# Optimization experiments

Measured on AMD Instinct MI355X. Metric: run time of the kernel, lower is better.

Reference implementation:

```python
import jax, jax.numpy as jnp
import numpy as np

HEADS = 8
DIM_HEAD = 64
SCALE = DIM_HEAD ** -0.5


def setup_inputs() -> dict:
    key = jax.random.key(0)
    ks = jax.random.split(key, 8)
    B, Nq, Dq = 4, 2048, 512
    Nk, Dc = 1024, 768
    inner = HEADS * DIM_HEAD  # 512
    x = jax.random.normal(ks[0], (B, Nq, Dq), dtype=jnp.float32)
    context = jax.random.normal(ks[1], (B, Nk, Dc), dtype=jnp.float32)
    # Linear weights stored [in, out]; y = x @ W (+ b)
    Wq = jax.random.normal(ks[2], (Dq, inner), dtype=jnp.float32) / np.sqrt(Dq)
    Wk = jax.random.normal(ks[3], (Dc, inner), dtype=jnp.float32) / np.sqrt(Dc)
    Wv = jax.random.normal(ks[4], (Dc, inner), dtype=jnp.float32) / np.sqrt(Dc)
    Wo = jax.random.normal(ks[5], (inner, Dq), dtype=jnp.float32) / np.sqrt(inner)
    bo = jax.random.normal(ks[6], (Dq,), dtype=jnp.float32) * 0.01
    return {"x": x, "context": context, "Wq": Wq, "Wk": Wk, "Wv": Wv, "Wo": Wo, "bo": bo}


def reference(x, context, Wq, Wk, Wv, Wo, bo):
    B, Nq, _ = x.shape
    Nk = context.shape[1]
    # projections
    q = x @ Wq          # [B, Nq, h*d]
    k = context @ Wk    # [B, Nk, h*d]
    v = context @ Wv    # [B, Nk, h*d]
    # split heads: b n (h d) -> b h n d
    q = q.reshape(B, Nq, HEADS, DIM_HEAD).transpose(0, 2, 1, 3)
    k = k.reshape(B, Nk, HEADS, DIM_HEAD).transpose(0, 2, 1, 3)
    v = v.reshape(B, Nk, HEADS, DIM_HEAD).transpose(0, 2, 1, 3)
    # fp32 QK^T (ATTN_PRECISION == 'fp32' path)
    sim = jnp.einsum('bhid,bhjd->bhij', q.astype(jnp.float32), k.astype(jnp.float32)) * SCALE
    attn = jax.nn.softmax(sim, axis=-1)
    out = jnp.einsum('bhij,bhjd->bhid', attn, v)  # [B, h, Nq, d]
    out = out.transpose(0, 2, 1, 3).reshape(B, Nq, HEADS * DIM_HEAD)
    return out @ Wo + bo  # dropout=0 -> identity
```

## Files before the change

kernel.cpp:

```cpp
#include <hip/hip_runtime.h>
#include <cstddef>
#include <cstdint>

typedef __attribute__((ext_vector_type(8))) short bf16x8;
typedef __attribute__((ext_vector_type(4))) float f32x4;

static __device__ __forceinline__ short f2bf(float f) {
    union { float f; unsigned u; } x;
    x.f = f;
    unsigned r = (x.u + 0x7FFFu + ((x.u >> 16) & 1u)) >> 16;
    return (short)r;
}

typedef __attribute__((address_space(3))) unsigned lds_u;
typedef const __attribute__((address_space(1))) unsigned glb_u;
static __device__ __forceinline__ void gld_lds16(const void* g, void* l) {
    __builtin_amdgcn_global_load_lds((glb_u*)g, (lds_u*)l, 16, 0, 0);
}

__global__ __launch_bounds__(256) void convert_kernel(
    const float* __restrict__ x, const float* __restrict__ c,
    short* __restrict__ xb, short* __restrict__ cb, int n1, int n2)
{
    int i = blockIdx.x * 256 + threadIdx.x;
    int nn1 = n1 >> 2;
    const float* src; short* dst; int off;
    if (i < nn1) { src = x; dst = xb; off = i; }
    else { src = c; dst = cb; off = i - nn1; if (off >= (n2 >> 2)) return; }
    float4 v = ((const float4*)src)[off];
    ushort4 w;
    w.x = (unsigned short)f2bf(v.x); w.y = (unsigned short)f2bf(v.y);
    w.z = (unsigned short)f2bf(v.z); w.w = (unsigned short)f2bf(v.w);
    ((ushort4*)dst)[off] = w;
}

__global__ __launch_bounds__(256) void wtrans_kernel(
    const float* __restrict__ Wq, const float* __restrict__ Wk,
    const float* __restrict__ Wv, const float* __restrict__ Wo,
    short* __restrict__ wqT, short* __restrict__ wkvT, short* __restrict__ woT)
{
    __shared__ float T[32][33];
    const int z = blockIdx.z;
    const float* src; short* dst; int R;
    if (z == 0)      { src = Wq; dst = wqT;  R = 512; }
    else if (z == 1) { src = Wk; dst = wkvT; R = 768; }
    else if (z == 2) { src = Wv; dst = wkvT + (size_t)512 * 768; R = 768; }
    else             { src = Wo; dst = woT;  R = 512; }
    const int yt = blockIdx.y;
    if (yt * 32 >= R) return;
    const int xt = blockIdx.x;
    const int tid = threadIdx.x;
    {
        int r = tid >> 3, c4 = (tid & 7) * 4;
        float4 v = *(const float4*)&src[(size_t)(yt * 32 + r) * 512 + xt * 32 + c4];
        T[r][c4] = v.x; T[r][c4 + 1] = v.y; T[r][c4 + 2] = v.z; T[r][c4 + 3] = v.w;
    }
    __syncthreads();
    {
        int cc = tid >> 3, r4 = (tid & 7) * 4;
        ushort4 w;
        w.x = (unsigned short)f2bf(T[r4][cc]);     w.y = (unsigned short)f2bf(T[r4 + 1][cc]);
        w.z = (unsigned short)f2bf(T[r4 + 2][cc]); w.w = (unsigned short)f2bf(T[r4 + 3][cc]);
        *(ushort4*)&dst[(size_t)(xt * 32 + cc) * R + yt * 32 + r4] = w;
    }
}

__global__ __launch_bounds__(256) void vtrans_kernel(
    const short* __restrict__ v, short* __restrict__ vT)
{
    __shared__ short T[32][33];
    const int b = blockIdx.z, yt = blockIdx.y, xt = blockIdx.x;
    const int tid = threadIdx.x;
    {
        int r = tid >> 3, c4 = (tid & 7) * 4;
        ushort4 vv = *(const ushort4*)&v[((size_t)(b * 1024 + yt * 32 + r)) * 1024 + xt * 32 + c4];
        T[r][c4] = (short)vv.x; T[r][c4 + 1] = (short)vv.y;
        T[r][c4 + 2] = (short)vv.z; T[r][c4 + 3] = (short)vv.w;
    }
    __syncthreads();
    {
        int cc = tid >> 3, r4 = (tid & 7) * 4;
        ushort4 w;
        w.x = (unsigned short)T[r4][cc];     w.y = (unsigned short)T[r4 + 1][cc];
        w.z = (unsigned short)T[r4 + 2][cc]; w.w = (unsigned short)T[r4 + 3][cc];
        *(ushort4*)&vT[((size_t)(b * 512 + xt * 32 + cc)) * 1024 + yt * 32 + r4] = w;
    }
}

static __device__ __forceinline__ void gemm_core(
    const short* __restrict__ A, const short* __restrict__ BT, int K,
    int bm, int bn, short* As, short* Bs, f32x4 acc[4][4])
{
    const int tid  = threadIdx.x;
    const int lane = tid & 63;
    const int wave = tid >> 6;
    const int lm   = lane & 15;
    const int quad = lane >> 4;
    const int wm = (wave >> 1) * 64;
    const int wn = (wave & 1) * 64;
    const int c = tid >> 7, r = tid & 127;

    {
        const short* Ag = &A[(size_t)(bm + r) * K];
        const short* Bg = &BT[(size_t)(bn + r) * K];
        gld_lds16(Ag + c * 8,       &As[tid * 8]);
        gld_lds16(Ag + (c + 2) * 8, &As[(tid + 256) * 8]);
        gld_lds16(Bg + c * 8,       &Bs[tid * 8]);
        gld_lds16(Bg + (c + 2) * 8, &Bs[(tid + 256) * 8]);
    }

    for (int k0 = 0, it = 0; k0 < K; k0 += 32, ++it) {
        short* Ac = As + (it & 1) * 4096;
        short* Bc = Bs + (it & 1) * 4096;
        __syncthreads();
        if (k0 + 32 < K) {
            short* An = As + ((it & 1) ^ 1) * 4096;
            short* Bn = Bs + ((it & 1) ^ 1) * 4096;
            const short* Ag = &A[(size_t)(bm + r) * K + k0 + 32];
            const short* Bg = &BT[(size_t)(bn + r) * K + k0 + 32];
            gld_lds16(Ag + c * 8,       &An[tid * 8]);
            gld_lds16(Ag + (c + 2) * 8, &An[(tid + 256) * 8]);
            gld_lds16(Bg + c * 8,       &Bn[tid * 8]);
            gld_lds16(Bg + (c + 2) * 8, &Bn[(tid + 256) * 8]);
        }
        bf16x8 af[4], bfr[4];
        #pragma unroll
        for (int i = 0; i < 4; ++i)
            af[i] = *(const bf16x8*)&Ac[(quad * 128 + wm + i * 16 + lm) * 8];
        #pragma unroll
        for (int j = 0; j < 4; ++j)
            bfr[j] = *(const bf16x8*)&Bc[(quad * 128 + wn + j * 16 + lm) * 8];
        #pragma unroll
        for (int i = 0; i < 4; ++i)
            #pragma unroll
            for (int j = 0; j < 4; ++j)
                acc[i][j] = __builtin_amdgcn_mfma_f32_16x16x32_bf16(
                    af[i], bfr[j], acc[i][j], 0, 0, 0);
    }
}

__global__ __launch_bounds__(256) void qkv_kernel(
    const short* __restrict__ xb, const short* __restrict__ cb,
    const short* __restrict__ wqT, const short* __restrict__ wkvT,
    short* __restrict__ qb, short* __restrict__ kvb)
{
    __shared__ short As[2 * 4096];
    __shared__ short Bs[2 * 4096];
    const int bid = blockIdx.x;
    const short *A, *BT; short* C; int K, ldc, bm, bn;
    if (bid < 256) { A = xb; BT = wqT;  C = qb;  K = 512; ldc = 512;
                     bm = (bid >> 2) * 128; bn = (bid & 3) * 128; }
    else { int b2 = bid - 256; A = cb; BT = wkvT; C = kvb; K = 768; ldc = 1024;
           bm = (b2 >> 3) * 128; bn = (b2 & 7) * 128; }

    f32x4 acc[4][4] = {};
    gemm_core(A, BT, K, bm, bn, As, Bs, acc);

    const int lane = threadIdx.x & 63, wave = threadIdx.x >> 6;
    const int lm = lane & 15, quad = lane >> 4;
    const int wm = (wave >> 1) * 64, wn = (wave & 1) * 64;
    #pragma unroll
    for (int j = 0; j < 4; ++j) {
        int col = bn + wn + j * 16 + lm;
        #pragma unroll
        for (int i = 0; i < 4; ++i) {
            int row0 = bm + wm + i * 16 + quad * 4;
            #pragma unroll
            for (int r = 0; r < 4; ++r)
                C[(size_t)(row0 + r) * ldc + col] = f2bf(acc[i][j][r]);
        }
    }
}

__global__ __launch_bounds__(256) void ogemm_kernel(
    const short* __restrict__ ob, const short* __restrict__ woT,
    const float* __restrict__ bias, float* __restrict__ out)
{
    __shared__ short As[2 * 4096];
    __shared__ short Bs[2 * 4096];
    const int bid = blockIdx.x;
    const int bm = (bid >> 2) * 128, bn = (bid & 3) * 128;

    f32x4 acc[4][4] = {};
    gemm_core(ob, woT, 512, bm, bn, As, Bs, acc);

    const int lane = threadIdx.x & 63, wave = threadIdx.x >> 6;
    const int lm = lane & 15, quad = lane >> 4;
    const int wm = (wave >> 1) * 64, wn = (wave & 1) * 64;
    #pragma unroll
    for (int j = 0; j < 4; ++j) {
        int col = bn + wn + j * 16 + lm;
        float bv = bias[col];
        #pragma unroll
        for (int i = 0; i < 4; ++i) {
            int row0 = bm + wm + i * 16 + quad * 4;
            #pragma unroll
            for (int r = 0; r < 4; ++r)
                out[(size_t)(row0 + r) * 512 + col] = acc[i][j][r] + bv;
        }
    }
}

__global__ __launch_bounds__(256) void attn_kernel(
    const short* __restrict__ q, const short* __restrict__ k,
    const short* __restrict__ vT, short* __restrict__ o)
{
    __shared__ short Qs[4096];
    __shared__ short Ks[2 * 4096];
    __shared__ short Vs[2 * 4096];

    const int tid  = threadIdx.x;
    const int lane = tid & 63;
    const int wave = tid >> 6;
    const int lm   = lane & 15;
    const int quad = lane >> 4;
    const int qt = blockIdx.x, h = blockIdx.y, b = blockIdx.z;
    const size_t qrow0 = (size_t)b * 2048 + qt * 64;
    const size_t krow0 = (size_t)b * 1024;
    const int hcol = h * 64;
    const size_t vrow0 = ((size_t)b * 8 + h) * 64;
    const int sc = tid >> 6, sr = tid & 63;

    #pragma unroll
    for (int p = 0; p < 2; ++p) {
        int idx = p * 256 + tid;
        int c = idx >> 6, r = idx & 63;
        gld_lds16(&q[(qrow0 + r) * 512 + hcol + c * 8], &Qs[idx * 8]);
        gld_lds16(&k[(krow0 + r) * 1024 + hcol + c * 8], &Ks[idx * 8]);
        gld_lds16(&vT[(vrow0 + r) * 1024 + c * 8], &Vs[idx * 8]);
    }
    __syncthreads();
    bf16x8 qf0 = *(const bf16x8*)&Qs[((0 + quad) * 64 + wave * 16 + lm) * 8];
    bf16x8 qf1 = *(const bf16x8*)&Qs[((4 + quad) * 64 + wave * 16 + lm) * 8];

    short* Pw = &Qs[wave * 1024];
    const int pr0 = lm * 64 + ((quad ^ (lm & 7)) << 3);
    const int pr1 = lm * 64 + (((quad + 4) ^ (lm & 7)) << 3);

    constexpr float C1 = 0.18033688f;
    constexpr float C2 = 11.5415603f;

    f32x4 oacc[4] = {};
    float lrow[4] = {0.0f, 0.0f, 0.0f, 0.0f};

    for (int t = 0; t < 16; ++t) {
        const short* Kc = &Ks[(t & 1) * 4096];
        const short* Vc = &Vs[(t & 1) * 4096];
        __syncthreads();
        if (t + 1 < 16) {
            short* Kn = &Ks[((t & 1) ^ 1) * 4096];
            short* Vn = &Vs[((t & 1) ^ 1) * 4096];
            #pragma unroll
            for (int p = 0; p < 2; ++p) {
                int idx = p * 256 + tid;
                int c = idx >> 6, r = idx & 63;
                gld_lds16(&k[(krow0 + (t + 1) * 64 + r) * 1024 + hcol + c * 8], &Kn[idx * 8]);
                gld_lds16(&vT[(vrow0 + r) * 1024 + (t + 1) * 64 + c * 8], &Vn[idx * 8]);
            }
        }

        f32x4 sacc[4] = {};
        #pragma unroll
        for (int j = 0; j < 4; ++j) {
            bf16x8 kf0 = *(const bf16x8*)&Kc[((0 + quad) * 64 + j * 16 + lm) * 8];
            bf16x8 kf1 = *(const bf16x8*)&Kc[((4 + quad) * 64 + j * 16 + lm) * 8];
            sacc[j] = __builtin_amdgcn_mfma_f32_16x16x32_bf16(qf0, kf0, sacc[j], 0, 0, 0);
            sacc[j] = __builtin_amdgcn_mfma_f32_16x16x32_bf16(qf1, kf1, sacc[j], 0, 0, 0);
        }

        #pragma unroll
        for (int r = 0; r < 4; ++r) {
            int row = quad * 4 + r;
            int rsw = (row & 7);
            float lsum = 0.0f;
            #pragma unroll
            for (int j = 0; j < 4; ++j) {
                float pv = exp2f(fmaf(sacc[j][r], C1, -C2));
                lsum += pv;
                int cc = (2 * j + (lm >> 3)) ^ rsw;
                Pw[row * 64 + (cc << 3) + (lm & 7)] = f2bf(pv);
            }
            lrow[r] += lsum;
        }
        bf16x8 pf0 = *(const bf16x8*)&Pw[pr0];
        bf16x8 pf1 = *(const bf16x8*)&Pw[pr1];

        #pragma unroll
        for (int j = 0; j < 4; ++j) {
            bf16x8 vf0 = *(const bf16x8*)&Vc[((0 + quad) * 64 + j * 16 + lm) * 8];
            bf16x8 vf1 = *(const bf16x8*)&Vc[((4 + quad) * 64 + j * 16 + lm) * 8];
            oacc[j] = __builtin_amdgcn_mfma_f32_16x16x32_bf16(pf0, vf0, oacc[j], 0, 0, 0);
            oacc[j] = __builtin_amdgcn_mfma_f32_16x16x32_bf16(pf1, vf1, oacc[j], 0, 0, 0);
        }
    }

    float inv[4];
    #pragma unroll
    for (int r = 0; r < 4; ++r) {
        float s = lrow[r];
        #pragma unroll
        for (int d = 1; d < 16; d <<= 1) s += __shfl_xor(s, d);
        inv[r] = 1.0f / s;
    }
    #pragma unroll
    for (int j = 0; j < 4; ++j) {
        int col = hcol + j * 16 + lm;
        #pragma unroll
        for (int r = 0; r < 4; ++r) {
            size_t row = qrow0 + wave * 16 + quad * 4 + r;
            o[row * 512 + col] = f2bf(oacc[j][r] * inv[r]);
        }
    }
}

extern "C" void kernel_launch(void* const* d_in, const int* in_sizes, int n_in,
                              void* d_out, int out_size, void* d_ws, size_t ws_size,
                              hipStream_t stream)
{
    const float* x   = (const float*)d_in[0];
    const float* ctx = (const float*)d_in[1];
    const float* Wq  = (const float*)d_in[2];
    const float* Wk  = (const float*)d_in[3];
    const float* Wv  = (const float*)d_in[4];
    const float* Wo  = (const float*)d_in[5];
    const float* bo  = (const float*)d_in[6];

    char* ws = (char*)d_ws;
    short* xb   = (short*)(ws);
    short* cb   = (short*)(ws + (8u << 20));
    short* wqT  = (short*)(ws + (14u << 20));
    short* wkvT = (short*)(ws + (14u << 20) + (512u << 10));
    short* woT  = (short*)(ws + (16u << 20));
    short* qb   = (short*)(ws + (16u << 20) + (512u << 10));
    short* kvb  = (short*)(ws + (24u << 20) + (512u << 10));
    short* ob   = xb;
    short* vT   = cb;

    convert_kernel<<<7168, 256, 0, stream>>>(x, ctx, xb, cb, 8192 * 512, 4096 * 768);
    wtrans_kernel<<<dim3(16, 24, 4), 256, 0, stream>>>(Wq, Wk, Wv, Wo, wqT, wkvT, woT);
    qkv_kernel<<<512, 256, 0, stream>>>(xb, cb, wqT, wkvT, qb, kvb);
    vtrans_kernel<<<dim3(16, 32, 4), 256, 0, stream>>>(kvb + 512, vT);
    attn_kernel<<<dim3(32, 8, 4), 256, 0, stream>>>(qb, kvb, vT, ob);
    ogemm_kernel<<<256, 256, 0, stream>>>(ob, woT, bo, (float*)d_out);
}
```

Measured before the change: 184.8 us.

## Merge prep kernels, retile GEMMs to 64x128 with K=64, double attention query tile

The conversion and weight-transpose kernels are merged into one launch. The projection GEMMs now use 64x128 tiles with a 64-wide K step, giving twice as many blocks with launch-bounds hints for occupancy. The attention kernel now handles 128 query rows per block, reusing each K/V tile across two query subtiles, and uses a cheaper round-half-up bf16 conversion for the probabilities. Risks include higher LDS and register pressure, and fewer attention blocks (512) to spread across the CUs.

```diff
diff --git a/kernel.cpp b/kernel.cpp
--- a/kernel.cpp
+++ b/kernel.cpp
@@ -11,6 +11,11 @@
     unsigned r = (x.u + 0x7FFFu + ((x.u >> 16) & 1u)) >> 16;
     return (short)r;
 }
+static __device__ __forceinline__ short f2bf_fast(float f) {
+    union { float f; unsigned u; } x;
+    x.f = f;
+    return (short)((x.u + 0x8000u) >> 16);
+}
 
 typedef __attribute__((address_space(3))) unsigned lds_u;
 typedef const __attribute__((address_space(1))) unsigned glb_u;
@@ -18,38 +23,36 @@
     __builtin_amdgcn_global_load_lds((glb_u*)g, (lds_u*)l, 16, 0, 0);
 }
 
-__global__ __launch_bounds__(256) void convert_kernel(
+__global__ __launch_bounds__(256) void prep_kernel(
     const float* __restrict__ x, const float* __restrict__ c,
-    short* __restrict__ xb, short* __restrict__ cb, int n1, int n2)
-{
-    int i = blockIdx.x * 256 + threadIdx.x;
-    int nn1 = n1 >> 2;
-    const float* src; short* dst; int off;
-    if (i < nn1) { src = x; dst = xb; off = i; }
-    else { src = c; dst = cb; off = i - nn1; if (off >= (n2 >> 2)) return; }
-    float4 v = ((const float4*)src)[off];
-    ushort4 w;
-    w.x = (unsigned short)f2bf(v.x); w.y = (unsigned short)f2bf(v.y);
-    w.z = (unsigned short)f2bf(v.z); w.w = (unsigned short)f2bf(v.w);
-    ((ushort4*)dst)[off] = w;
-}
-
-__global__ __launch_bounds__(256) void wtrans_kernel(
     const float* __restrict__ Wq, const float* __restrict__ Wk,
     const float* __restrict__ Wv, const float* __restrict__ Wo,
+    short* __restrict__ xb, short* __restrict__ cb,
     short* __restrict__ wqT, short* __restrict__ wkvT, short* __restrict__ woT)
 {
+    const int bid = blockIdx.x;
+    const int tid = threadIdx.x;
+    if (bid < 7168) {
+        int i = bid * 256 + tid;
+        int nn1 = (8192 * 512) >> 2;
+        const float* src; short* dst; int off;
+        if (i < nn1) { src = x; dst = xb; off = i; }
+        else { src = c; dst = cb; off = i - nn1; }
+        float4 v = ((const float4*)src)[off];
+        ushort4 w;
+        w.x = (unsigned short)f2bf(v.x); w.y = (unsigned short)f2bf(v.y);
+        w.z = (unsigned short)f2bf(v.z); w.w = (unsigned short)f2bf(v.w);
+        ((ushort4*)dst)[off] = w;
+        return;
+    }
     __shared__ float T[32][33];
-    const int z = blockIdx.z;
-    const float* src; short* dst; int R;
-    if (z == 0)      { src = Wq; dst = wqT;  R = 512; }
-    else if (z == 1) { src = Wk; dst = wkvT; R = 768; }
-    else if (z == 2) { src = Wv; dst = wkvT + (size_t)512 * 768; R = 768; }
-    else             { src = Wo; dst = woT;  R = 512; }
-    const int yt = blockIdx.y;
-    if (yt * 32 >= R) return;
-    const int xt = blockIdx.x;
-    const int tid = threadIdx.x;
+    int w = bid - 7168;
+    const float* src; short* dst; int R, t;
+    if (w < 256)       { src = Wq; dst = wqT;  R = 512; t = w; }
+    else if (w < 640)  { src = Wk; dst = wkvT; R = 768; t = w - 256; }
+    else if (w < 1024) { src = Wv; dst = wkvT + (size_t)512 * 768; R = 768; t = w - 640; }
+    else               { src = Wo; dst = woT;  R = 512; t = w - 1024; }
+    const int xt = t & 15, yt = t >> 4;
     {
         int r = tid >> 3, c4 = (tid & 7) * 4;
         float4 v = *(const float4*)&src[(size_t)(yt * 32 + r) * 512 + xt * 32 + c4];
@@ -58,10 +61,10 @@
     __syncthreads();
     {
         int cc = tid >> 3, r4 = (tid & 7) * 4;
-        ushort4 w;
-        w.x = (unsigned short)f2bf(T[r4][cc]);     w.y = (unsigned short)f2bf(T[r4 + 1][cc]);
-        w.z = (unsigned short)f2bf(T[r4 + 2][cc]); w.w = (unsigned short)f2bf(T[r4 + 3][cc]);
-        *(ushort4*)&dst[(size_t)(xt * 32 + cc) * R + yt * 32 + r4] = w;
+        ushort4 o;
+        o.x = (unsigned short)f2bf(T[r4][cc]);     o.y = (unsigned short)f2bf(T[r4 + 1][cc]);
+        o.z = (unsigned short)f2bf(T[r4 + 2][cc]); o.w = (unsigned short)f2bf(T[r4 + 3][cc]);
+        *(ushort4*)&dst[(size_t)(xt * 32 + cc) * R + yt * 32 + r4] = o;
     }
 }
 
@@ -87,83 +90,90 @@
     }
 }
 
-static __device__ __forceinline__ void gemm_core(
+static __device__ __forceinline__ void gemm_core64(
     const short* __restrict__ A, const short* __restrict__ BT, int K,
-    int bm, int bn, short* As, short* Bs, f32x4 acc[4][4])
+    int bm, int bn, short* As, short* Bs, f32x4 acc[2][4])
 {
     const int tid  = threadIdx.x;
     const int lane = tid & 63;
     const int wave = tid >> 6;
     const int lm   = lane & 15;
     const int quad = lane >> 4;
-    const int wm = (wave >> 1) * 64;
+    const int wm = (wave >> 1) * 32;
     const int wn = (wave & 1) * 64;
-    const int c = tid >> 7, r = tid & 127;
-
-    {
-        const short* Ag = &A[(size_t)(bm + r) * K];
-        const short* Bg = &BT[(size_t)(bn + r) * K];
-        gld_lds16(Ag + c * 8,       &As[tid * 8]);
-        gld_lds16(Ag + (c + 2) * 8, &As[(tid + 256) * 8]);
-        gld_lds16(Bg + c * 8,       &Bs[tid * 8]);
-        gld_lds16(Bg + (c + 2) * 8, &Bs[(tid + 256) * 8]);
-    }
-
-    for (int k0 = 0, it = 0; k0 < K; k0 += 32, ++it) {
+    const int ca = tid >> 6, ra = tid & 63;
+    const int cb = tid >> 7, rb = tid & 127;
+
+    {
+        const short* Ag = &A[(size_t)(bm + ra) * K];
+        gld_lds16(Ag + ca * 8,       &As[(ca * 64 + ra) * 8]);
+        gld_lds16(Ag + (ca + 4) * 8, &As[((ca + 4) * 64 + ra) * 8]);
+        const short* Bg = &BT[(size_t)(bn + rb) * K];
+        #pragma unroll
+        for (int p = 0; p < 4; ++p)
+            gld_lds16(Bg + (cb + 2 * p) * 8, &Bs[((cb + 2 * p) * 128 + rb) * 8]);
+    }
+
+    const int nit = K >> 6;
+    for (int it = 0; it < nit; ++it) {
         short* Ac = As + (it & 1) * 4096;
-        short* Bc = Bs + (it & 1) * 4096;
+        short* Bc = Bs + (it & 1) * 8192;
         __syncthreads();
-        if (k0 + 32 < K) {
-            short* An = As + ((it & 1) ^ 1) * 4096;
-            short* Bn = Bs + ((it & 1) ^ 1) * 4096;
-            const short* Ag = &A[(size_t)(bm + r) * K + k0 + 32];
-            const short* Bg = &BT[(size_t)(bn + r) * K + k0 + 32];
-            gld_lds16(Ag + c * 8,       &An[tid * 8]);
-            gld_lds16(Ag + (c + 2) * 8, &An[(tid + 256) * 8]);
-            gld_lds16(Bg + c * 8,       &Bn[tid * 8]);
-            gld_lds16(Bg + (c + 2) * 8, &Bn[(tid + 256) * 8]);
-        }
-        bf16x8 af[4], bfr[4];
-        #pragma unroll
-        for (int i = 0; i < 4; ++i)
-            af[i] = *(const bf16x8*)&Ac[(quad * 128 + wm + i * 16 + lm) * 8];
-        #pragma unroll
-        for (int j = 0; j < 4; ++j)
-            bfr[j] = *(const bf16x8*)&Bc[(quad * 128 + wn + j * 16 + lm) * 8];
-        #pragma unroll
-        for (int i = 0; i < 4; ++i)
+        if (it + 1 < nit) {
+            short* An = As + ((it + 1) & 1) * 4096;
+            short* Bn = Bs + ((it + 1) & 1) * 8192;
+            const short* Ag = &A[(size_t)(bm + ra) * K + (it + 1) * 64];
+            gld_lds16(Ag + ca * 8,       &An[(ca * 64 + ra) * 8]);
+            gld_lds16(Ag + (ca + 4) * 8, &An[((ca + 4) * 64 + ra) * 8]);
+            const short* Bg = &BT[(size_t)(bn + rb) * K + (it + 1) * 64];
+            #pragma unroll
+            for (int p = 0; p < 4; ++p)
+                gld_lds16(Bg + (cb + 2 * p) * 8, &Bn[((cb + 2 * p) * 128 + rb) * 8]);
+        }
+        #pragma unroll
+        for (int h = 0; h < 2; ++h) {
+            bf16x8 af[2], bfr[4];
+            #pragma unroll
+            for (int i = 0; i < 2; ++i)
+                af[i] = *(const bf16x8*)&Ac[((h * 4 + quad) * 64 + wm + i * 16 + lm) * 8];
             #pragma unroll
             for (int j = 0; j < 4; ++j)
-                acc[i][j] = __builtin_amdgcn_mfma_f32_16x16x32_bf16(
-                    af[i], bfr[j], acc[i][j], 0, 0, 0);
-    }
-}
-
-__global__ __launch_bounds__(256) void qkv_kernel(
+                bfr[j] = *(const bf16x8*)&Bc[((h * 4 + quad) * 128 + wn + j * 16 + lm) * 8];
+            #pragma unroll
+            for (int i = 0; i < 2; ++i)
+                #pragma unroll
+                for (int j = 0; j < 4; ++j)
+                    acc[i][j] = __builtin_amdgcn_mfma_f32_16x16x32_bf16(
+                        af[i], bfr[j], acc[i][j], 0, 0, 0);
+        }
+    }
+}
+
+__global__ __launch_bounds__(256, 3) void qkv_kernel(
     const short* __restrict__ xb, const short* __restrict__ cb,
     const short* __restrict__ wqT, const short* __restrict__ wkvT,
     short* __restrict__ qb, short* __restrict__ kvb)
 {
     __shared__ short As[2 * 4096];
-    __shared__ short Bs[2 * 4096];
+    __shared__ short Bs[2 * 8192];
     const int bid = blockIdx.x;
     const short *A, *BT; short* C; int K, ldc, bm, bn;
-    if (bid < 256) { A = xb; BT = wqT;  C = qb;  K = 512; ldc = 512;
-                     bm = (bid >> 2) * 128; bn = (bid & 3) * 128; }
-    else { int b2 = bid - 256; A = cb; BT = wkvT; C = kvb; K = 768; ldc = 1024;
-           bm = (b2 >> 3) * 128; bn = (b2 & 7) * 128; }
-
-    f32x4 acc[4][4] = {};
-    gemm_core(A, BT, K, bm, bn, As, Bs, acc);
+    if (bid < 512) { A = xb; BT = wqT;  C = qb;  K = 512; ldc = 512;
+                     bm = (bid >> 2) * 64; bn = (bid & 3) * 128; }
+    else { int b2 = bid - 512; A = cb; BT = wkvT; C = kvb; K = 768; ldc = 1024;
+           bm = (b2 >> 3) * 64; bn = (b2 & 7) * 128; }
+
+    f32x4 acc[2][4] = {};
+    gemm_core64(A, BT, K, bm, bn, As, Bs, acc);
 
     const int lane = threadIdx.x & 63, wave = threadIdx.x >> 6;
     const int lm = lane & 15, quad = lane >> 4;
-    const int wm = (wave >> 1) * 64, wn = (wave & 1) * 64;
+    const int wm = (wave >> 1) * 32, wn = (wave & 1) * 64;
     #pragma unroll
     for (int j = 0; j < 4; ++j) {
         int col = bn + wn + j * 16 + lm;
         #pragma unroll
-        for (int i = 0; i < 4; ++i) {
+        for (int i = 0; i < 2; ++i) {
             int row0 = bm + wm + i * 16 + quad * 4;
             #pragma unroll
             for (int r = 0; r < 4; ++r)
@@ -172,27 +182,27 @@
     }
 }
 
-__global__ __launch_bounds__(256) void ogemm_kernel(
+__global__ __launch_bounds__(256, 3) void ogemm_kernel(
     const short* __restrict__ ob, const short* __restrict__ woT,
     const float* __restrict__ bias, float* __restrict__ out)
 {
     __shared__ short As[2 * 4096];
-    __shared__ short Bs[2 * 4096];
+    __shared__ short Bs[2 * 8192];
     const int bid = blockIdx.x;
-    const int bm = (bid >> 2) * 128, bn = (bid & 3) * 128;
-
-    f32x4 acc[4][4] = {};
-    gemm_core(ob, woT, 512, bm, bn, As, Bs, acc);
+    const int bm = (bid >> 2) * 64, bn = (bid & 3) * 128;
+
+    f32x4 acc[2][4] = {};
+    gemm_core64(ob, woT, 512, bm, bn, As, Bs, acc);
 
     const int lane = threadIdx.x & 63, wave = threadIdx.x >> 6;
     const int lm = lane & 15, quad = lane >> 4;
-    const int wm = (wave >> 1) * 64, wn = (wave & 1) * 64;
+    const int wm = (wave >> 1) * 32, wn = (wave & 1) * 64;
     #pragma unroll
     for (int j = 0; j < 4; ++j) {
         int col = bn + wn + j * 16 + lm;
         float bv = bias[col];
         #pragma unroll
-        for (int i = 0; i < 4; ++i) {
+        for (int i = 0; i < 2; ++i) {
             int row0 = bm + wm + i * 16 + quad * 4;
             #pragma unroll
             for (int r = 0; r < 4; ++r)
@@ -201,11 +211,11 @@
     }
 }
 
-__global__ __launch_bounds__(256) void attn_kernel(
+__global__ __launch_bounds__(256, 3) void attn_kernel(
     const short* __restrict__ q, const short* __restrict__ k,
     const short* __restrict__ vT, short* __restrict__ o)
 {
-    __shared__ short Qs[4096];
+    __shared__ short Qs[8192];
     __shared__ short Ks[2 * 4096];
     __shared__ short Vs[2 * 4096];
 
@@ -215,41 +225,63 @@
     const int lm   = lane & 15;
     const int quad = lane >> 4;
     const int qt = blockIdx.x, h = blockIdx.y, b = blockIdx.z;
-    const size_t qrow0 = (size_t)b * 2048 + qt * 64;
+    const size_t qrow0 = (size_t)b * 2048 + qt * 128;
     const size_t krow0 = (size_t)b * 1024;
     const int hcol = h * 64;
     const size_t vrow0 = ((size_t)b * 8 + h) * 64;
-    const int sc = tid >> 6, sr = tid & 63;
-
+
+    #pragma unroll
+    for (int p = 0; p < 4; ++p) {
+        int idx = p * 256 + tid;
+        int u = idx >> 9, c = (idx >> 6) & 7, r = idx & 63;
+        gld_lds16(&q[(qrow0 + u * 64 + r) * 512 + hcol + c * 8], &Qs[idx * 8]);
+    }
     #pragma unroll
     for (int p = 0; p < 2; ++p) {
         int idx = p * 256 + tid;
         int c = idx >> 6, r = idx & 63;
-        gld_lds16(&q[(qrow0 + r) * 512 + hcol + c * 8], &Qs[idx * 8]);
         gld_lds16(&k[(krow0 + r) * 1024 + hcol + c * 8], &Ks[idx * 8]);
         gld_lds16(&vT[(vrow0 + r) * 1024 + c * 8], &Vs[idx * 8]);
     }
     __syncthreads();
-    bf16x8 qf0 = *(const bf16x8*)&Qs[((0 + quad) * 64 + wave * 16 + lm) * 8];
-    bf16x8 qf1 = *(const bf16x8*)&Qs[((4 + quad) * 64 + wave * 16 + lm) * 8];
-
-    short* Pw = &Qs[wave * 1024];
-    const int pr0 = lm * 64 + ((quad ^ (lm & 7)) << 3);
-    const int pr1 = lm * 64 + (((quad + 4) ^ (lm & 7)) << 3);
+    bf16x8 qf[2][2];
+    #pragma unroll
+    for (int u = 0; u < 2; ++u)
+        #pragma unroll
+        for (int hf = 0; hf < 2; ++hf)
+            qf[u][hf] = *(const bf16x8*)&Qs[u * 4096 +
+                         ((hf * 4 + quad) * 64 + wave * 16 + lm) * 8];
+
+    const int pb0 = (0 * 4 + wave) * 1024;
+    const int pb1 = (1 * 4 + wave) * 1024;
+    int rowo[4], swz[4];
+    #pragma unroll
+    for (int r = 0; r < 4; ++r) {
+        int row = quad * 4 + r;
+        rowo[r] = row * 64 + (lm & 7);
+        swz[r]  = row & 7;
+    }
+    int pr[2][2];
+    #pragma unroll
+    for (int u = 0; u < 2; ++u)
+        #pragma unroll
+        for (int hf = 0; hf < 2; ++hf)
+            pr[u][hf] = (u * 4 + wave) * 1024 + lm * 64 +
+                        (((hf * 4 + quad) ^ (lm & 7)) << 3);
 
     constexpr float C1 = 0.18033688f;
     constexpr float C2 = 11.5415603f;
 
-    f32x4 oacc[4] = {};
-    float lrow[4] = {0.0f, 0.0f, 0.0f, 0.0f};
+    f32x4 oacc[2][4] = {};
+    float lrow[2][4] = {};
 
     for (int t = 0; t < 16; ++t) {
         const short* Kc = &Ks[(t & 1) * 4096];
         const short* Vc = &Vs[(t & 1) * 4096];
         __syncthreads();
         if (t + 1 < 16) {
-            short* Kn = &Ks[((t & 1) ^ 1) * 4096];
-            short* Vn = &Vs[((t & 1) ^ 1) * 4096];
+            short* Kn = &Ks[((t + 1) & 1) * 4096];
+            short* Vn = &Vs[((t + 1) & 1) * 4096];
             #pragma unroll
             for (int p = 0; p < 2; ++p) {
                 int idx = p * 256 + tid;
@@ -259,56 +291,72 @@
             }
         }
 
-        f32x4 sacc[4] = {};
+        bf16x8 kf[4][2];
+        #pragma unroll
+        for (int j = 0; j < 4; ++j)
+            #pragma unroll
+            for (int hf = 0; hf < 2; ++hf)
+                kf[j][hf] = *(const bf16x8*)&Kc[((hf * 4 + quad) * 64 + j * 16 + lm) * 8];
+
+        #pragma unroll
+        for (int u = 0; u < 2; ++u) {
+            f32x4 sacc[4] = {};
+            #pragma unroll
+            for (int j = 0; j < 4; ++j) {
+                sacc[j] = __builtin_amdgcn_mfma_f32_16x16x32_bf16(qf[u][0], kf[j][0], sacc[j], 0, 0, 0);
+                sacc[j] = __builtin_amdgcn_mfma_f32_16x16x32_bf16(qf[u][1], kf[j][1], sacc[j], 0, 0, 0);
+            }
+            const int pb = u ? pb1 : pb0;
+            #pragma unroll
+            for (int r = 0; r < 4; ++r) {
+                float lsum = 0.0f;
+                #pragma unroll
+                for (int j = 0; j < 4; ++j) {
+                    float pv = exp2f(fmaf(sacc[j][r], C1, -C2));
+                    lsum += pv;
+                    int cc = (2 * j + (lm >> 3)) ^ swz[r];
+                    Qs[pb + rowo[r] + (cc << 3)] = f2bf_fast(pv);
+                }
+                lrow[u][r] += lsum;
+            }
+        }
+
+        bf16x8 vf[4][2];
+        #pragma unroll
+        for (int j = 0; j < 4; ++j)
+            #pragma unroll
+            for (int hf = 0; hf < 2; ++hf)
+                vf[j][hf] = *(const bf16x8*)&Vc[((hf * 4 + quad) * 64 + j * 16 + lm) * 8];
+        #pragma unroll
+        for (int u = 0; u < 2; ++u) {
+            bf16x8 pf0 = *(const bf16x8*)&Qs[pr[u][0]];
+            bf16x8 pf1 = *(const bf16x8*)&Qs[pr[u][1]];
+            #pragma unroll
+            for (int j = 0; j < 4; ++j) {
+                oacc[u][j] = __builtin_amdgcn_mfma_f32_16x16x32_bf16(pf0, vf[j][0], oacc[u][j], 0, 0, 0);
+                oacc[u][j] = __builtin_amdgcn_mfma_f32_16x16x32_bf16(pf1, vf[j][1], oacc[u][j], 0, 0, 0);
+            }
+        }
+    }
+
+    #pragma unroll
+    for (int u = 0; u < 2; ++u) {
+        float inv[4];
+        #pragma unroll
+        for (int r = 0; r < 4; ++r) {
+            float s = lrow[u][r];
+            #pragma unroll
+            for (int d = 1; d < 16; d <<= 1) s += __shfl_xor(s, d);
+            inv[r] = 1.0f / s;
+        }
         #pragma unroll
         for (int j = 0; j < 4; ++j) {
-            bf16x8 kf0 = *(const bf16x8*)&Kc[((0 + quad) * 64 + j * 16 + lm) * 8];
-            bf16x8 kf1 = *(const bf16x8*)&Kc[((4 + quad) * 64 + j * 16 + lm) * 8];
-            sacc[j] = __builtin_amdgcn_mfma_f32_16x16x32_bf16(qf0, kf0, sacc[j], 0, 0, 0);
-            sacc[j] = __builtin_amdgcn_mfma_f32_16x16x32_bf16(qf1, kf1, sacc[j], 0, 0, 0);
-        }
-
-        #pragma unroll
-        for (int r = 0; r < 4; ++r) {
-            int row = quad * 4 + r;
-            int rsw = (row & 7);
-            float lsum = 0.0f;
-            #pragma unroll
-            for (int j = 0; j < 4; ++j) {
-                float pv = exp2f(fmaf(sacc[j][r], C1, -C2));
-                lsum += pv;
-                int cc = (2 * j + (lm >> 3)) ^ rsw;
-                Pw[row * 64 + (cc << 3) + (lm & 7)] = f2bf(pv);
-            }
-            lrow[r] += lsum;
-        }
-        bf16x8 pf0 = *(const bf16x8*)&Pw[pr0];
-        bf16x8 pf1 = *(const bf16x8*)&Pw[pr1];
-
-        #pragma unroll
-        for (int j = 0; j < 4; ++j) {
-            bf16x8 vf0 = *(const bf16x8*)&Vc[((0 + quad) * 64 + j * 16 + lm) * 8];
-            bf16x8 vf1 = *(const bf16x8*)&Vc[((4 + quad) * 64 + j * 16 + lm) * 8];
-            oacc[j] = __builtin_amdgcn_mfma_f32_16x16x32_bf16(pf0, vf0, oacc[j], 0, 0, 0);
-            oacc[j] = __builtin_amdgcn_mfma_f32_16x16x32_bf16(pf1, vf1, oacc[j], 0, 0, 0);
-        }
-    }
-
-    float inv[4];
-    #pragma unroll
-    for (int r = 0; r < 4; ++r) {
-        float s = lrow[r];
-        #pragma unroll
-        for (int d = 1; d < 16; d <<= 1) s += __shfl_xor(s, d);
-        inv[r] = 1.0f / s;
-    }
-    #pragma unroll
-    for (int j = 0; j < 4; ++j) {
-        int col = hcol + j * 16 + lm;
-        #pragma unroll
-        for (int r = 0; r < 4; ++r) {
-            size_t row = qrow0 + wave * 16 + quad * 4 + r;
-            o[row * 512 + col] = f2bf(oacc[j][r] * inv[r]);
+            int col = hcol + j * 16 + lm;
+            #pragma unroll
+            for (int r = 0; r < 4; ++r) {
+                size_t row = qrow0 + u * 64 + wave * 16 + quad * 4 + r;
+                o[row * 512 + col] = f2bf(oacc[u][j][r] * inv[r]);
+            }
         }
     }
 }
@@ -336,10 +384,10 @@
     short* ob   = xb;
     short* vT   = cb;
 
-    convert_kernel<<<7168, 256, 0, stream>>>(x, ctx, xb, cb, 8192 * 512, 4096 * 768);
-    wtrans_kernel<<<dim3(16, 24, 4), 256, 0, stream>>>(Wq, Wk, Wv, Wo, wqT, wkvT, woT);
-    qkv_kernel<<<512, 256, 0, stream>>>(xb, cb, wqT, wkvT, qb, kvb);
+    prep_kernel<<<8448, 256, 0, stream>>>(x, ctx, Wq, Wk, Wv, Wo,
+                                          xb, cb, wqT, wkvT, woT);
+    qkv_kernel<<<1024, 256, 0, stream>>>(xb, cb, wqT, wkvT, qb, kvb);
     vtrans_kernel<<<dim3(16, 32, 4), 256, 0, stream>>>(kvb + 512, vT);
-    attn_kernel<<<dim3(32, 8, 4), 256, 0, stream>>>(qb, kvb, vT, ob);
-    ogemm_kernel<<<256, 256, 0, stream>>>(ob, woT, bo, (float*)d_out);
-}
+    attn_kernel<<<dim3(16, 8, 4), 256, 0, stream>>>(qb, kvb, vT, ob);
+    ogemm_kernel<<<512, 256, 0, stream>>>(ob, woT, bo, (float*)d_out);
+}
```

After: 205.9 us. 11.4% more time.

## Merge prep kernels, load GEMM fragments directly to registers, use fast bf16 rounding

Applied to the files above, without the earlier changes.

Fuses the input conversion and weight transpose kernels into one launch to save a kernel launch. Replaces the LDS double-buffered GEMM core with per-wave direct global-to-register fragment loads with software prefetch, using 256x64 tiles so each wave owns 64 rows. Switches the P-matrix bf16 conversion in attention to a cheaper round-half-up. Skipping LDS removes barriers, but the global loads are now strided (16 bytes per row) and B tiles are loaded redundantly by all four waves, which relies on L2/L1 for reuse.

```diff
diff --git a/kernel.cpp b/kernel.cpp
--- a/kernel.cpp
+++ b/kernel.cpp
@@ -11,6 +11,11 @@
     unsigned r = (x.u + 0x7FFFu + ((x.u >> 16) & 1u)) >> 16;
     return (short)r;
 }
+static __device__ __forceinline__ short f2bf_fast(float f) {
+    union { float f; unsigned u; } x;
+    x.f = f;
+    return (short)((x.u + 0x8000u) >> 16);
+}
 
 typedef __attribute__((address_space(3))) unsigned lds_u;
 typedef const __attribute__((address_space(1))) unsigned glb_u;
@@ -18,38 +23,36 @@
     __builtin_amdgcn_global_load_lds((glb_u*)g, (lds_u*)l, 16, 0, 0);
 }
 
-__global__ __launch_bounds__(256) void convert_kernel(
+__global__ __launch_bounds__(256) void prep_kernel(
     const float* __restrict__ x, const float* __restrict__ c,
-    short* __restrict__ xb, short* __restrict__ cb, int n1, int n2)
-{
-    int i = blockIdx.x * 256 + threadIdx.x;
-    int nn1 = n1 >> 2;
-    const float* src; short* dst; int off;
-    if (i < nn1) { src = x; dst = xb; off = i; }
-    else { src = c; dst = cb; off = i - nn1; if (off >= (n2 >> 2)) return; }
-    float4 v = ((const float4*)src)[off];
-    ushort4 w;
-    w.x = (unsigned short)f2bf(v.x); w.y = (unsigned short)f2bf(v.y);
-    w.z = (unsigned short)f2bf(v.z); w.w = (unsigned short)f2bf(v.w);
-    ((ushort4*)dst)[off] = w;
-}
-
-__global__ __launch_bounds__(256) void wtrans_kernel(
     const float* __restrict__ Wq, const float* __restrict__ Wk,
     const float* __restrict__ Wv, const float* __restrict__ Wo,
+    short* __restrict__ xb, short* __restrict__ cb,
     short* __restrict__ wqT, short* __restrict__ wkvT, short* __restrict__ woT)
 {
+    const int bid = blockIdx.x;
+    const int tid = threadIdx.x;
+    if (bid < 7168) {
+        int i = bid * 256 + tid;
+        int nn1 = (8192 * 512) >> 2;
+        const float* src; short* dst; int off;
+        if (i < nn1) { src = x; dst = xb; off = i; }
+        else { src = c; dst = cb; off = i - nn1; }
+        float4 v = ((const float4*)src)[off];
+        ushort4 w;
+        w.x = (unsigned short)f2bf(v.x); w.y = (unsigned short)f2bf(v.y);
+        w.z = (unsigned short)f2bf(v.z); w.w = (unsigned short)f2bf(v.w);
+        ((ushort4*)dst)[off] = w;
+        return;
+    }
     __shared__ float T[32][33];
-    const int z = blockIdx.z;
-    const float* src; short* dst; int R;
-    if (z == 0)      { src = Wq; dst = wqT;  R = 512; }
-    else if (z == 1) { src = Wk; dst = wkvT; R = 768; }
-    else if (z == 2) { src = Wv; dst = wkvT + (size_t)512 * 768; R = 768; }
-    else             { src = Wo; dst = woT;  R = 512; }
-    const int yt = blockIdx.y;
-    if (yt * 32 >= R) return;
-    const int xt = blockIdx.x;
-    const int tid = threadIdx.x;
+    int w = bid - 7168;
+    const float* src; short* dst; int R, t;
+    if (w < 256)       { src = Wq; dst = wqT;  R = 512; t = w; }
+    else if (w < 640)  { src = Wk; dst = wkvT; R = 768; t = w - 256; }
+    else if (w < 1024) { src = Wv; dst = wkvT + (size_t)512 * 768; R = 768; t = w - 640; }
+    else               { src = Wo; dst = woT;  R = 512; t = w - 1024; }
+    const int xt = t & 15, yt = t >> 4;
     {
         int r = tid >> 3, c4 = (tid & 7) * 4;
         float4 v = *(const float4*)&src[(size_t)(yt * 32 + r) * 512 + xt * 32 + c4];
@@ -58,10 +61,10 @@
     __syncthreads();
     {
         int cc = tid >> 3, r4 = (tid & 7) * 4;
-        ushort4 w;
-        w.x = (unsigned short)f2bf(T[r4][cc]);     w.y = (unsigned short)f2bf(T[r4 + 1][cc]);
-        w.z = (unsigned short)f2bf(T[r4 + 2][cc]); w.w = (unsigned short)f2bf(T[r4 + 3][cc]);
-        *(ushort4*)&dst[(size_t)(xt * 32 + cc) * R + yt * 32 + r4] = w;
+        ushort4 o;
+        o.x = (unsigned short)f2bf(T[r4][cc]);     o.y = (unsigned short)f2bf(T[r4 + 1][cc]);
+        o.z = (unsigned short)f2bf(T[r4 + 2][cc]); o.w = (unsigned short)f2bf(T[r4 + 3][cc]);
+        *(ushort4*)&dst[(size_t)(xt * 32 + cc) * R + yt * 32 + r4] = o;
     }
 }
 
@@ -87,55 +90,43 @@
     }
 }
 
-static __device__ __forceinline__ void gemm_core(
+static __device__ __forceinline__ void gemm_reg_core(
     const short* __restrict__ A, const short* __restrict__ BT, int K,
-    int bm, int bn, short* As, short* Bs, f32x4 acc[4][4])
-{
-    const int tid  = threadIdx.x;
-    const int lane = tid & 63;
-    const int wave = tid >> 6;
-    const int lm   = lane & 15;
-    const int quad = lane >> 4;
-    const int wm = (wave >> 1) * 64;
-    const int wn = (wave & 1) * 64;
-    const int c = tid >> 7, r = tid & 127;
-
-    {
-        const short* Ag = &A[(size_t)(bm + r) * K];
-        const short* Bg = &BT[(size_t)(bn + r) * K];
-        gld_lds16(Ag + c * 8,       &As[tid * 8]);
-        gld_lds16(Ag + (c + 2) * 8, &As[(tid + 256) * 8]);
-        gld_lds16(Bg + c * 8,       &Bs[tid * 8]);
-        gld_lds16(Bg + (c + 2) * 8, &Bs[(tid + 256) * 8]);
-    }
-
-    for (int k0 = 0, it = 0; k0 < K; k0 += 32, ++it) {
-        short* Ac = As + (it & 1) * 4096;
-        short* Bc = Bs + (it & 1) * 4096;
-        __syncthreads();
-        if (k0 + 32 < K) {
-            short* An = As + ((it & 1) ^ 1) * 4096;
-            short* Bn = Bs + ((it & 1) ^ 1) * 4096;
-            const short* Ag = &A[(size_t)(bm + r) * K + k0 + 32];
-            const short* Bg = &BT[(size_t)(bn + r) * K + k0 + 32];
-            gld_lds16(Ag + c * 8,       &An[tid * 8]);
-            gld_lds16(Ag + (c + 2) * 8, &An[(tid + 256) * 8]);
-            gld_lds16(Bg + c * 8,       &Bn[tid * 8]);
-            gld_lds16(Bg + (c + 2) * 8, &Bn[(tid + 256) * 8]);
-        }
-        bf16x8 af[4], bfr[4];
-        #pragma unroll
-        for (int i = 0; i < 4; ++i)
-            af[i] = *(const bf16x8*)&Ac[(quad * 128 + wm + i * 16 + lm) * 8];
-        #pragma unroll
-        for (int j = 0; j < 4; ++j)
-            bfr[j] = *(const bf16x8*)&Bc[(quad * 128 + wn + j * 16 + lm) * 8];
+    int bm, int bn, f32x4 acc[4][4])
+{
+    const int lane = threadIdx.x & 63;
+    const int wave = threadIdx.x >> 6;
+    const int lm = lane & 15, quad = lane >> 4;
+
+    const short* Ab = A  + (size_t)(bm + wave * 64 + lm) * K + quad * 8;
+    const short* Bb = BT + (size_t)(bn + lm) * K + quad * 8;
+    const size_t rsA = (size_t)16 * K;
+    const size_t rsB = (size_t)16 * K;
+
+    bf16x8 af[4], bfr[4], afn[4], bfn[4];
+    #pragma unroll
+    for (int i = 0; i < 4; ++i) af[i]  = *(const bf16x8*)(Ab + i * rsA);
+    #pragma unroll
+    for (int j = 0; j < 4; ++j) bfr[j] = *(const bf16x8*)(Bb + j * rsB);
+
+    const int nit = K >> 5;
+    for (int it = 0; it < nit; ++it) {
+        if (it + 1 < nit) {
+            const short* An = Ab + (it + 1) * 32;
+            const short* Bn = Bb + (it + 1) * 32;
+            #pragma unroll
+            for (int i = 0; i < 4; ++i) afn[i] = *(const bf16x8*)(An + i * rsA);
+            #pragma unroll
+            for (int j = 0; j < 4; ++j) bfn[j] = *(const bf16x8*)(Bn + j * rsB);
+        }
         #pragma unroll
         for (int i = 0; i < 4; ++i)
             #pragma unroll
             for (int j = 0; j < 4; ++j)
                 acc[i][j] = __builtin_amdgcn_mfma_f32_16x16x32_bf16(
                     af[i], bfr[j], acc[i][j], 0, 0, 0);
+        #pragma unroll
+        for (int i = 0; i < 4; ++i) { af[i] = afn[i]; bfr[i] = bfn[i]; }
     }
 }
 
@@ -144,27 +135,24 @@
     const short* __restrict__ wqT, const short* __restrict__ wkvT,
     short* __restrict__ qb, short* __restrict__ kvb)
 {
-    __shared__ short As[2 * 4096];
-    __shared__ short Bs[2 * 4096];
     const int bid = blockIdx.x;
     const short *A, *BT; short* C; int K, ldc, bm, bn;
     if (bid < 256) { A = xb; BT = wqT;  C = qb;  K = 512; ldc = 512;
-                     bm = (bid >> 2) * 128; bn = (bid & 3) * 128; }
+                     bm = (bid >> 3) * 256; bn = (bid & 7) * 64; }
     else { int b2 = bid - 256; A = cb; BT = wkvT; C = kvb; K = 768; ldc = 1024;
-           bm = (b2 >> 3) * 128; bn = (b2 & 7) * 128; }
+           bm = (b2 >> 4) * 256; bn = (b2 & 15) * 64; }
 
     f32x4 acc[4][4] = {};
-    gemm_core(A, BT, K, bm, bn, As, Bs, acc);
+    gemm_reg_core(A, BT, K, bm, bn, acc);
 
     const int lane = threadIdx.x & 63, wave = threadIdx.x >> 6;
     const int lm = lane & 15, quad = lane >> 4;
-    const int wm = (wave >> 1) * 64, wn = (wave & 1) * 64;
     #pragma unroll
     for (int j = 0; j < 4; ++j) {
-        int col = bn + wn + j * 16 + lm;
+        int col = bn + j * 16 + lm;
         #pragma unroll
         for (int i = 0; i < 4; ++i) {
-            int row0 = bm + wm + i * 16 + quad * 4;
+            int row0 = bm + wave * 64 + i * 16 + quad * 4;
             #pragma unroll
             for (int r = 0; r < 4; ++r)
                 C[(size_t)(row0 + r) * ldc + col] = f2bf(acc[i][j][r]);
@@ -176,24 +164,21 @@
     const short* __restrict__ ob, const short* __restrict__ woT,
     const float* __restrict__ bias, float* __restrict__ out)
 {
-    __shared__ short As[2 * 4096];
-    __shared__ short Bs[2 * 4096];
     const int bid = blockIdx.x;
-    const int bm = (bid >> 2) * 128, bn = (bid & 3) * 128;
+    const int bm = (bid >> 3) * 256, bn = (bid & 7) * 64;
 
     f32x4 acc[4][4] = {};
-    gemm_core(ob, woT, 512, bm, bn, As, Bs, acc);
+    gemm_reg_core(ob, woT, 512, bm, bn, acc);
 
     const int lane = threadIdx.x & 63, wave = threadIdx.x >> 6;
     const int lm = lane & 15, quad = lane >> 4;
-    const int wm = (wave >> 1) * 64, wn = (wave & 1) * 64;
     #pragma unroll
     for (int j = 0; j < 4; ++j) {
-        int col = bn + wn + j * 16 + lm;
+        int col = bn + j * 16 + lm;
         float bv = bias[col];
         #pragma unroll
         for (int i = 0; i < 4; ++i) {
-            int row0 = bm + wm + i * 16 + quad * 4;
+            int row0 = bm + wave * 64 + i * 16 + quad * 4;
             #pragma unroll
             for (int r = 0; r < 4; ++r)
                 out[(size_t)(row0 + r) * 512 + col] = acc[i][j][r] + bv;
@@ -219,7 +204,6 @@
     const size_t krow0 = (size_t)b * 1024;
     const int hcol = h * 64;
     const size_t vrow0 = ((size_t)b * 8 + h) * 64;
-    const int sc = tid >> 6, sr = tid & 63;
 
     #pragma unroll
     for (int p = 0; p < 2; ++p) {
@@ -248,8 +232,8 @@
         const short* Vc = &Vs[(t & 1) * 4096];
         __syncthreads();
         if (t + 1 < 16) {
-            short* Kn = &Ks[((t & 1) ^ 1) * 4096];
-            short* Vn = &Vs[((t & 1) ^ 1) * 4096];
+            short* Kn = &Ks[((t + 1) & 1) * 4096];
+            short* Vn = &Vs[((t + 1) & 1) * 4096];
             #pragma unroll
             for (int p = 0; p < 2; ++p) {
                 int idx = p * 256 + tid;
@@ -278,7 +262,7 @@
                 float pv = exp2f(fmaf(sacc[j][r], C1, -C2));
                 lsum += pv;
                 int cc = (2 * j + (lm >> 3)) ^ rsw;
-                Pw[row * 64 + (cc << 3) + (lm & 7)] = f2bf(pv);
+                Pw[row * 64 + (cc << 3) + (lm & 7)] = f2bf_fast(pv);
             }
             lrow[r] += lsum;
         }
@@ -336,8 +320,8 @@
     short* ob   = xb;
     short* vT   = cb;
 
-    convert_kernel<<<7168, 256, 0, stream>>>(x, ctx, xb, cb, 8192 * 512, 4096 * 768);
-    wtrans_kernel<<<dim3(16, 24, 4), 256, 0, stream>>>(Wq, Wk, Wv, Wo, wqT, wkvT, woT);
+    prep_kernel<<<8448, 256, 0, stream>>>(x, ctx, Wq, Wk, Wv, Wo,
+                                          xb, cb, wqT, wkvT, woT);
     qkv_kernel<<<512, 256, 0, stream>>>(xb, cb, wqT, wkvT, qb, kvb);
     vtrans_kernel<<<dim3(16, 32, 4), 256, 0, stream>>>(kvb + 512, vT);
     attn_kernel<<<dim3(32, 8, 4), 256, 0, stream>>>(qb, kvb, vT, ob);
```

After: 199.5 us. 1.08x slower.
